# Kernel tuning notes

Hardware: AMD Instinct MI355X
Metric: run time of the kernel (lower is better)

Reference implementation:

```python
import jax, jax.numpy as jnp
import numpy as np
from math import sqrt

B, S, I, H, O, R = 32, 2048, 128, 512, 64, 1
ALPHA = 0.1


def setup_inputs() -> dict:
    key = jax.random.key(0)
    ks = jax.random.split(key, 7)
    x = jax.random.normal(ks[0], (B, S, I), dtype=jnp.float32)
    input_projective = jax.random.normal(ks[1], (H, R), dtype=jnp.float32) / sqrt(H)
    input_receptive = jax.random.normal(ks[2], (I, R), dtype=jnp.float32) / sqrt(I)
    rec_projective = jax.random.normal(ks[3], (H, R), dtype=jnp.float32) / sqrt(H)
    rec_receptive = jax.random.normal(ks[4], (H, R), dtype=jnp.float32) / sqrt(H)
    bound = 1.0 / sqrt(H)
    readout_w = jax.random.uniform(ks[5], (O, H), minval=-bound, maxval=bound, dtype=jnp.float32)
    readout_b = jax.random.uniform(ks[6], (O,), minval=-bound, maxval=bound, dtype=jnp.float32)
    return {
        "x": x,
        "input_projective": input_projective,
        "input_receptive": input_receptive,
        "rec_projective": rec_projective,
        "rec_receptive": rec_receptive,
        "readout_w": readout_w,
        "readout_b": readout_b,
    }


def reference(x, input_projective, input_receptive, rec_projective, rec_receptive, readout_w, readout_b):
    # Precompute input drive for all steps using the low-rank factorization:
    # x_in[b,s,h] = x[b,s,:] @ input_receptive @ input_projective.T
    x_in = jnp.einsum("bsi,ir,hr->bsh", x, input_receptive, input_projective)

    def step(h, xin_t):
        # r_in = (J @ h.T).T with J = P @ R.T  ->  h @ R @ P.T (low-rank)
        r_in = (h @ rec_receptive) @ rec_projective.T
        dh = -h + jax.nn.relu(r_in + xin_t)  # activation = nlfun (relu)
        h = h + ALPHA * dh                   # Euler hidden update
        out_t = h @ readout_w.T + readout_b
        return h, out_t

    h0 = jnp.zeros((x.shape[0], rec_projective.shape[0]), dtype=x.dtype)
    _, out = jax.lax.scan(step, h0, jnp.swapaxes(x_in, 0, 1))  # scan over time
    return jnp.swapaxes(out, 0, 1)  # [B, S, O]
```

## Files before the change

### kernel.cpp

```cpp
#include <hip/hip_runtime.h>


#define B_ 32
#define S_ 2048
#define I_ 128
#define H_ 512
#define O_ 64

typedef __attribute__((ext_vector_type(8))) short bf16x8;
typedef __attribute__((ext_vector_type(4))) float f32x4;

__device__ __forceinline__ unsigned short f2bf(float f) {
  unsigned int b = __float_as_uint(f);
  b += 0x7FFFu + ((b >> 16) & 1u);
  return (unsigned short)(b >> 16);
}
__device__ __forceinline__ float bf2f(unsigned short s) {
  return __uint_as_float(((unsigned)s) << 16);
}
__device__ __forceinline__ unsigned pack_bf(float lo, float hi) {
  unsigned a = (__float_as_uint(lo) + 0x8000u) >> 16;
  unsigned b = (__float_as_uint(hi) + 0x8000u) & 0xFFFF0000u;
  return a | b;
}

#define DPP_ADD(s, CTRL) \
  s += __int_as_float(__builtin_amdgcn_update_dpp(0, __float_as_int(s), CTRL, 0xF, 0xF, true))

#define RL(s, L) __int_as_float(__builtin_amdgcn_readlane(__float_as_int(s), (L)))

__device__ __forceinline__ void gload16(const void* g, void* l) {
  __builtin_amdgcn_global_load_lds(
      (const __attribute__((address_space(1))) unsigned int*)g,
      (__attribute__((address_space(3))) unsigned int*)l, 16, 0, 0);
}
#define WAITVM(N) asm volatile("s_waitcnt vmcnt(" #N ")" ::: "memory")
#define SCHEDB() __builtin_amdgcn_sched_barrier(0)

#define OFF_SU 0
#define OFF_SV 1920
#define OFF_RP 3456
#define OFF_IP 5504
#define OFF_SW 7552
#define OFF_XS 48512
#define SMEM_BYTES 146816

__device__ __forceinline__ int swz(int row, int col) {
  return row * 64 + (col ^ ((((unsigned)row >> 2) & 3) << 4));
}

__global__ __launch_bounds__(512, 1) void k_fused(
    const float* __restrict__ x, const float* __restrict__ ipj,
    const float* __restrict__ irc, const float* __restrict__ rpj,
    const float* __restrict__ rrc, const float* __restrict__ Wr,
    const float* __restrict__ bias, float* __restrict__ out) {
  extern __shared__ __align__(16) char smem[];
  float* su = (float*)(smem + OFF_SU);
  float* sV = (float*)(smem + OFF_SV);
  float* srp = (float*)(smem + OFF_RP);
  float* sip = (float*)(smem + OFF_IP);
  unsigned short* sw = (unsigned short*)(smem + OFF_SW);
  unsigned short* sBF = (unsigned short*)(smem + OFF_XS);
  float* xsf = (float*)(smem + OFF_XS);

  const int tid = threadIdx.x;
  const int wv = tid >> 6;
  const int lane = tid & 63;
  const int b = blockIdx.x >> 3;
  const int g = blockIdx.x & 7;
  const int r0 = g * 256;

  f32x4 cv0 = *(const f32x4*)(irc + 4 * (lane & 7));
  f32x4 cv1 = *(const f32x4*)(irc + 4 * (lane & 7) + 32);
  f32x4 cv2 = *(const f32x4*)(irc + 4 * (lane & 7) + 64);
  f32x4 cv3 = *(const f32x4*)(irc + 4 * (lane & 7) + 96);
  float rpv[8], ipv[8], rrv[8];
  #pragma unroll
  for (int k = 0; k < 8; k++) {
    int h = lane + 64 * k;
    rpv[k] = rpj[h]; ipv[k] = ipj[h]; rrv[k] = 0.1f * rrc[h];
  }
  if (tid < 96) su[384 + tid] = 0.f;
  if (tid < 80) sV[304 + tid] = 0.f;

#define ISSUE(c) do { \
    int tc_ = r0 - 128 + (c) * 64 + wv * 8; if (tc_ < 0) tc_ = 0; \
    const float* gs_ = x + ((size_t)b * S_ + tc_) * I_ + lane * 4; \
    char* ld_ = (char*)xsf + ((c) % 3) * 32768 + wv * 4096; \
    gload16(gs_,       ld_); \
    gload16(gs_ + 256, ld_ + 1024); \
    gload16(gs_ + 512, ld_ + 2048); \
    gload16(gs_ + 768, ld_ + 3072); \
  } while (0)

#define COMPUTE(c) do { \
    const float* bp_ = xsf + ((c) % 3) * 8192 + (wv * 8 + (lane >> 3)) * 128 + (lane & 7) * 4; \
    f32x4 x0_ = *(const f32x4*)(bp_); \
    f32x4 x1_ = *(const f32x4*)(bp_ + 32); \
    f32x4 x2_ = *(const f32x4*)(bp_ + 64); \
    f32x4 x3_ = *(const f32x4*)(bp_ + 96); \
    float p0_ = x0_[0] * cv0[0], p1_ = x0_[1] * cv0[1]; \
    float p2_ = x0_[2] * cv0[2], p3_ = x0_[3] * cv0[3]; \
    p0_ = fmaf(x1_[0], cv1[0], p0_); p1_ = fmaf(x1_[1], cv1[1], p1_); \
    p2_ = fmaf(x1_[2], cv1[2], p2_); p3_ = fmaf(x1_[3], cv1[3], p3_); \
    p0_ = fmaf(x2_[0], cv2[0], p0_); p1_ = fmaf(x2_[1], cv2[1], p1_); \
    p2_ = fmaf(x2_[2], cv2[2], p2_); p3_ = fmaf(x2_[3], cv2[3], p3_); \
    p0_ = fmaf(x3_[0], cv3[0], p0_); p1_ = fmaf(x3_[1], cv3[1], p1_); \
    p2_ = fmaf(x3_[2], cv3[2], p2_); p3_ = fmaf(x3_[3], cv3[3], p3_); \
    float s_ = (p0_ + p1_) + (p2_ + p3_); \
    DPP_ADD(s_, 0x121); DPP_ADD(s_, 0x122); DPP_ADD(s_, 0x124); \
    float mask_ = (r0 - 128 + (c) * 64 >= 0) ? 1.f : 0.f; \
    if ((lane & 7) == 7) su[(c) * 64 + wv * 8 + (lane >> 3)] = s_ * mask_; \
  } while (0)

  ISSUE(0); ISSUE(1); ISSUE(2);
  WAITVM(8); COMPUTE(0); SCHEDB(); ISSUE(3);
  WAITVM(8); COMPUTE(1); SCHEDB(); ISSUE(4);
  WAITVM(8); COMPUTE(2); SCHEDB(); ISSUE(5);
  WAITVM(8); COMPUTE(3);
  WAITVM(4); COMPUTE(4);
  WAITVM(0); COMPUTE(5);
  __syncthreads();

  if (wv < 4) {
    float suA = su[76 * wv + 32 + lane];
    float suB = su[76 * wv + 96 + lane];
#define VSTEP(UT) do { \
    float ut_ = (UT); \
    float q0 = fmaxf(fmaf(v, rpv[0], ut_ * ipv[0]), 0.f) * rrv[0]; \
    float q1 = fmaxf(fmaf(v, rpv[1], ut_ * ipv[1]), 0.f) * rrv[1]; \
    float q2 = fmaxf(fmaf(v, rpv[2], ut_ * ipv[2]), 0.f) * rrv[2]; \
    float q3 = fmaxf(fmaf(v, rpv[3], ut_ * ipv[3]), 0.f) * rrv[3]; \
    float q4 = fmaxf(fmaf(v, rpv[4], ut_ * ipv[4]), 0.f) * rrv[4]; \
    float q5 = fmaxf(fmaf(v, rpv[5], ut_ * ipv[5]), 0.f) * rrv[5]; \
    float q6 = fmaxf(fmaf(v, rpv[6], ut_ * ipv[6]), 0.f) * rrv[6]; \
    float q7 = fmaxf(fmaf(v, rpv[7], ut_ * ipv[7]), 0.f) * rrv[7]; \
    float s_ = ((q0 + q1) + (q2 + q3)) + ((q4 + q5) + (q6 + q7)); \
    DPP_ADD(s_, 0x121); DPP_ADD(s_, 0x122); DPP_ADD(s_, 0x124); DPP_ADD(s_, 0x128); \
    DPP_ADD(s_, 0x142); DPP_ADD(s_, 0x143); \
    float tot_ = RL(s_, 63); \
    v = fmaf(0.9f, v, tot_); \
  } while (0)
    float v = 0.f;
    int base = wv * 76;
    #pragma unroll 8
    for (int i = 0; i < 48; i++) VSTEP(RL(suA, i));
    #pragma unroll 8
    for (int k = 0; k < 16; k++) {
      if (lane == 0) sV[base + k] = v;
      VSTEP(RL(suA, 48 + k));
    }
    #pragma unroll 4
    for (int k = 16; k < 76; k++) {
      if (lane == 0) sV[base + k] = v;
      VSTEP(RL(suB, k - 16));
    }
  } else {
    int tid2 = tid - 256;
#define WSEG(m) do { \
    int seg_ = tid2 + 256 * (m); \
    int l2_ = seg_ & 63, ot_ = (seg_ >> 6) & 3, kt_ = seg_ >> 8; \
    const float4* wp_ = (const float4*)(Wr + (size_t)(ot_ * 16 + (l2_ & 15)) * H_ + kt_ * 32 + (l2_ >> 4) * 8); \
    float4 Wa_ = wp_[0], Wb_ = wp_[1]; \
    uint4 pk_; \
    pk_.x = (unsigned)f2bf(Wa_.x) | ((unsigned)f2bf(Wa_.y) << 16); \
    pk_.y = (unsigned)f2bf(Wa_.z) | ((unsigned)f2bf(Wa_.w) << 16); \
    pk_.z = (unsigned)f2bf(Wb_.x) | ((unsigned)f2bf(Wb_.y) << 16); \
    pk_.w = (unsigned)f2bf(Wb_.z) | ((unsigned)f2bf(Wb_.w) << 16); \
    *(uint4*)(sBF + seg_ * 8) = pk_; \
  } while (0)
    WSEG(0);  WSEG(1);  WSEG(2);  WSEG(3);
    WSEG(4);  WSEG(5);  WSEG(6);  WSEG(7);
    WSEG(8);  WSEG(9);  WSEG(10); WSEG(11);
    WSEG(12); WSEG(13); WSEG(14); WSEG(15);
    srp[tid2] = rpj[tid2]; srp[tid2 + 256] = rpj[tid2 + 256];
    sip[tid2] = ipj[tid2]; sip[tid2 + 256] = ipj[tid2 + 256];
  }
  __syncthreads();

  {
    int tl = lane & 15, quad = lane >> 4;
    float Vr0 = sV[(wv * 3 + 0) * 16 + tl], ur0 = su[80 + (wv * 3 + 0) * 16 + tl];
    float Vr1 = sV[(wv * 3 + 1) * 16 + tl], ur1 = su[80 + (wv * 3 + 1) * 16 + tl];
    float Vr2 = sV[(wv * 3 + 2) * 16 + tl], ur2 = su[80 + (wv * 3 + 2) * 16 + tl];
    f32x4 acc[3][4] = {};
    #pragma unroll 4
    for (int kt = 0; kt < 16; kt++) {
      int hbase = kt * 32 + quad * 8;
      f32x4 rp4a = *(const f32x4*)(srp + hbase);
      f32x4 rp4b = *(const f32x4*)(srp + hbase + 4);
      f32x4 ip4a = *(const f32x4*)(sip + hbase);
      f32x4 ip4b = *(const f32x4*)(sip + hbase + 4);
      bf16x8 bfr0 = *(const bf16x8*)(sBF + (((kt * 4 + 0) * 64 + lane) << 3));
      bf16x8 bfr1 = *(const bf16x8*)(sBF + (((kt * 4 + 1) * 64 + lane) << 3));
      bf16x8 bfr2 = *(const bf16x8*)(sBF + (((kt * 4 + 2) * 64 + lane) << 3));
      bf16x8 bfr3 = *(const bf16x8*)(sBF + (((kt * 4 + 3) * 64 + lane) << 3));
      #pragma unroll
      for (int m = 0; m < 3; m++) {
        float Vm = m == 0 ? Vr0 : (m == 1 ? Vr1 : Vr2);
        float um = m == 0 ? ur0 : (m == 1 ? ur1 : ur2);
        float q[8];
        #pragma unroll
        for (int j = 0; j < 4; j++) {
          q[j]     = fmaxf(fmaf(Vm, rp4a[j], um * ip4a[j]), 0.f);
          q[4 + j] = fmaxf(fmaf(Vm, rp4b[j], um * ip4b[j]), 0.f);
        }
        union { bf16x8 v; unsigned w[4]; } a;
        #pragma unroll
        for (int j = 0; j < 4; j++) a.w[j] = pack_bf(q[2 * j], q[2 * j + 1]);
        acc[m][0] = __builtin_amdgcn_mfma_f32_16x16x32_bf16(a.v, bfr0, acc[m][0], 0, 0, 0);
        acc[m][1] = __builtin_amdgcn_mfma_f32_16x16x32_bf16(a.v, bfr1, acc[m][1], 0, 0, 0);
        acc[m][2] = __builtin_amdgcn_mfma_f32_16x16x32_bf16(a.v, bfr2, acc[m][2], 0, 0, 0);
        acc[m][3] = __builtin_amdgcn_mfma_f32_16x16x32_bf16(a.v, bfr3, acc[m][3], 0, 0, 0);
      }
    }
    #pragma unroll
    for (int m = 0; m < 3; m++) {
      int mt = wv * 3 + m;
      if (mt < 19) {
        int rbase = mt * 16 + quad * 4;
        #pragma unroll
        for (int r = 0; r < 4; r++) {
          #pragma unroll
          for (int ot = 0; ot < 4; ot++)
            sw[swz(rbase + r, ot * 16 + tl)] = f2bf(acc[m][ot][r]);
        }
      }
    }
  }
  __syncthreads();

  {
    float y = 0.f;
    float bo = bias[lane];
    int k0 = wv * 32;
    float* ob = out + ((size_t)(b * S_ + r0 + k0)) * O_ + lane;
    #pragma unroll 8
    for (int i = 0; i < 48; i++)
      y = fmaf(0.9f, y, 0.1f * bf2f(sw[swz(k0 + i, lane)]));
    #pragma unroll 4
    for (int i = 0; i < 32; i++) {
      y = fmaf(0.9f, y, 0.1f * bf2f(sw[swz(k0 + 48 + i, lane)]));
      ob[(size_t)i * O_] = y + bo;
    }
  }
}

extern "C" void kernel_launch(void* const* d_in, const int* in_sizes, int n_in,
                              void* d_out, int out_size, void* d_ws, size_t ws_size,
                              hipStream_t stream) {
  const float* x   = (const float*)d_in[0];
  const float* ipj = (const float*)d_in[1];
  const float* irc = (const float*)d_in[2];
  const float* rpj = (const float*)d_in[3];
  const float* rrc = (const float*)d_in[4];
  const float* Wr  = (const float*)d_in[5];
  const float* br  = (const float*)d_in[6];
  float* out = (float*)d_out;

  static bool s_init = false;
  if (!s_init) {
    hipFuncSetAttribute((const void*)k_fused,
                        hipFuncAttributeMaxDynamicSharedMemorySize, SMEM_BYTES);
    s_init = true;
  }
  k_fused<<<dim3(256), dim3(512), SMEM_BYTES, stream>>>(x, ipj, irc, rpj, rrc,
                                                        Wr, br, out);
}
```

Before: 114.3 us.

## Fold scales into serial recurrence, use med3 clamp, inline DPP reduce and cvt_pk_bf16

The scalar recurrence now pre-multiplies the projective and input weights by 0.1*receptive, so the relu-then-scale becomes a single fmed3 clamp with sign-dependent bounds. The DPP reduction is written as inline v_add_f32_dpp asm, and bf16 packing uses the hardware v_cvt_pk_bf16_f32 instruction. The 0.1 factor in the readout scan moves to the output store. The warmup length of the serial scan drops from 48 to 32 steps, which shortens the latency-bound critical path but gives a shorter burn-in for each chunk's initial state and may reduce accuracy.

```diff
diff --git a/kernel.cpp b/kernel.cpp
--- a/kernel.cpp
+++ b/kernel.cpp
@@ -18,14 +18,23 @@
 __device__ __forceinline__ float bf2f(unsigned short s) {
   return __uint_as_float(((unsigned)s) << 16);
 }
-__device__ __forceinline__ unsigned pack_bf(float lo, float hi) {
-  unsigned a = (__float_as_uint(lo) + 0x8000u) >> 16;
-  unsigned b = (__float_as_uint(hi) + 0x8000u) & 0xFFFF0000u;
-  return a | b;
+__device__ __forceinline__ unsigned cvtpk(float lo, float hi) {
+  unsigned r;
+  asm("v_cvt_pk_bf16_f32 %0, %1, %2" : "=v"(r) : "v"(lo), "v"(hi));
+  return r;
 }
 
 #define DPP_ADD(s, CTRL) \
   s += __int_as_float(__builtin_amdgcn_update_dpp(0, __float_as_int(s), CTRL, 0xF, 0xF, true))
+
+#define DPP_RED(s) do { \
+  asm("v_add_f32_dpp %0, %0, %0 row_ror:1 row_mask:0xf bank_mask:0xf bound_ctrl:0" : "+v"(s)); \
+  asm("v_add_f32_dpp %0, %0, %0 row_ror:2 row_mask:0xf bank_mask:0xf bound_ctrl:0" : "+v"(s)); \
+  asm("v_add_f32_dpp %0, %0, %0 row_ror:4 row_mask:0xf bank_mask:0xf bound_ctrl:0" : "+v"(s)); \
+  asm("v_add_f32_dpp %0, %0, %0 row_ror:8 row_mask:0xf bank_mask:0xf bound_ctrl:0" : "+v"(s)); \
+  asm("v_add_f32_dpp %0, %0, %0 row_bcast:15 row_mask:0xa bank_mask:0xf" : "+v"(s)); \
+  asm("v_add_f32_dpp %0, %0, %0 row_bcast:31 row_mask:0xc bank_mask:0xf" : "+v"(s)); \
+} while (0)
 
 #define RL(s, L) __int_as_float(__builtin_amdgcn_readlane(__float_as_int(s), (L)))
 
@@ -74,11 +83,15 @@
   f32x4 cv1 = *(const f32x4*)(irc + 4 * (lane & 7) + 32);
   f32x4 cv2 = *(const f32x4*)(irc + 4 * (lane & 7) + 64);
   f32x4 cv3 = *(const f32x4*)(irc + 4 * (lane & 7) + 96);
-  float rpv[8], ipv[8], rrv[8];
+  float av[8], bv[8], lo_[8], hi_[8];
   #pragma unroll
   for (int k = 0; k < 8; k++) {
     int h = lane + 64 * k;
-    rpv[k] = rpj[h]; ipv[k] = ipj[h]; rrv[k] = 0.1f * rrc[h];
+    float rr = rrc[h], sc = 0.1f * rr;
+    av[k] = rpj[h] * sc;
+    bv[k] = ipj[h] * sc;
+    lo_[k] = rr > 0.f ? 0.f : -__builtin_inff();
+    hi_[k] = rr > 0.f ? __builtin_inff() : 0.f;
   }
   if (tid < 96) su[384 + tid] = 0.f;
   if (tid < 80) sV[304 + tid] = 0.f;
@@ -123,37 +136,44 @@
   __syncthreads();
 
   if (wv < 4) {
-    float suA = su[76 * wv + 32 + lane];
-    float suB = su[76 * wv + 96 + lane];
+    float suA = su[76 * wv + 48 + lane];
+    float suB = su[76 * wv + 112 + lane];
 #define VSTEP(UT) do { \
     float ut_ = (UT); \
-    float q0 = fmaxf(fmaf(v, rpv[0], ut_ * ipv[0]), 0.f) * rrv[0]; \
-    float q1 = fmaxf(fmaf(v, rpv[1], ut_ * ipv[1]), 0.f) * rrv[1]; \
-    float q2 = fmaxf(fmaf(v, rpv[2], ut_ * ipv[2]), 0.f) * rrv[2]; \
-    float q3 = fmaxf(fmaf(v, rpv[3], ut_ * ipv[3]), 0.f) * rrv[3]; \
-    float q4 = fmaxf(fmaf(v, rpv[4], ut_ * ipv[4]), 0.f) * rrv[4]; \
-    float q5 = fmaxf(fmaf(v, rpv[5], ut_ * ipv[5]), 0.f) * rrv[5]; \
-    float q6 = fmaxf(fmaf(v, rpv[6], ut_ * ipv[6]), 0.f) * rrv[6]; \
-    float q7 = fmaxf(fmaf(v, rpv[7], ut_ * ipv[7]), 0.f) * rrv[7]; \
+    float x0 = fmaf(v, av[0], ut_ * bv[0]); \
+    float x1 = fmaf(v, av[1], ut_ * bv[1]); \
+    float x2 = fmaf(v, av[2], ut_ * bv[2]); \
+    float x3 = fmaf(v, av[3], ut_ * bv[3]); \
+    float x4 = fmaf(v, av[4], ut_ * bv[4]); \
+    float x5 = fmaf(v, av[5], ut_ * bv[5]); \
+    float x6 = fmaf(v, av[6], ut_ * bv[6]); \
+    float x7 = fmaf(v, av[7], ut_ * bv[7]); \
+    float q0 = __builtin_amdgcn_fmed3f(x0, lo_[0], hi_[0]); \
+    float q1 = __builtin_amdgcn_fmed3f(x1, lo_[1], hi_[1]); \
+    float q2 = __builtin_amdgcn_fmed3f(x2, lo_[2], hi_[2]); \
+    float q3 = __builtin_amdgcn_fmed3f(x3, lo_[3], hi_[3]); \
+    float q4 = __builtin_amdgcn_fmed3f(x4, lo_[4], hi_[4]); \
+    float q5 = __builtin_amdgcn_fmed3f(x5, lo_[5], hi_[5]); \
+    float q6 = __builtin_amdgcn_fmed3f(x6, lo_[6], hi_[6]); \
+    float q7 = __builtin_amdgcn_fmed3f(x7, lo_[7], hi_[7]); \
     float s_ = ((q0 + q1) + (q2 + q3)) + ((q4 + q5) + (q6 + q7)); \
-    DPP_ADD(s_, 0x121); DPP_ADD(s_, 0x122); DPP_ADD(s_, 0x124); DPP_ADD(s_, 0x128); \
-    DPP_ADD(s_, 0x142); DPP_ADD(s_, 0x143); \
+    DPP_RED(s_); \
     float tot_ = RL(s_, 63); \
     v = fmaf(0.9f, v, tot_); \
   } while (0)
     float v = 0.f;
     int base = wv * 76;
     #pragma unroll 8
-    for (int i = 0; i < 48; i++) VSTEP(RL(suA, i));
+    for (int i = 0; i < 32; i++) VSTEP(RL(suA, i));
     #pragma unroll 8
-    for (int k = 0; k < 16; k++) {
+    for (int k = 0; k < 32; k++) {
       if (lane == 0) sV[base + k] = v;
-      VSTEP(RL(suA, 48 + k));
+      VSTEP(RL(suA, 32 + k));
     }
     #pragma unroll 4
-    for (int k = 16; k < 76; k++) {
+    for (int k = 32; k < 76; k++) {
       if (lane == 0) sV[base + k] = v;
-      VSTEP(RL(suB, k - 16));
+      VSTEP(RL(suB, k - 32));
     }
   } else {
     int tid2 = tid - 256;
@@ -163,10 +183,10 @@
     const float4* wp_ = (const float4*)(Wr + (size_t)(ot_ * 16 + (l2_ & 15)) * H_ + kt_ * 32 + (l2_ >> 4) * 8); \
     float4 Wa_ = wp_[0], Wb_ = wp_[1]; \
     uint4 pk_; \
-    pk_.x = (unsigned)f2bf(Wa_.x) | ((unsigned)f2bf(Wa_.y) << 16); \
-    pk_.y = (unsigned)f2bf(Wa_.z) | ((unsigned)f2bf(Wa_.w) << 16); \
-    pk_.z = (unsigned)f2bf(Wb_.x) | ((unsigned)f2bf(Wb_.y) << 16); \
-    pk_.w = (unsigned)f2bf(Wb_.z) | ((unsigned)f2bf(Wb_.w) << 16); \
+    pk_.x = cvtpk(Wa_.x, Wa_.y); \
+    pk_.y = cvtpk(Wa_.z, Wa_.w); \
+    pk_.z = cvtpk(Wb_.x, Wb_.y); \
+    pk_.w = cvtpk(Wb_.z, Wb_.w); \
     *(uint4*)(sBF + seg_ * 8) = pk_; \
   } while (0)
     WSEG(0);  WSEG(1);  WSEG(2);  WSEG(3);
@@ -207,7 +227,7 @@
         }
         union { bf16x8 v; unsigned w[4]; } a;
         #pragma unroll
-        for (int j = 0; j < 4; j++) a.w[j] = pack_bf(q[2 * j], q[2 * j + 1]);
+        for (int j = 0; j < 4; j++) a.w[j] = cvtpk(q[2 * j], q[2 * j + 1]);
         acc[m][0] = __builtin_amdgcn_mfma_f32_16x16x32_bf16(a.v, bfr0, acc[m][0], 0, 0, 0);
         acc[m][1] = __builtin_amdgcn_mfma_f32_16x16x32_bf16(a.v, bfr1, acc[m][1], 0, 0, 0);
         acc[m][2] = __builtin_amdgcn_mfma_f32_16x16x32_bf16(a.v, bfr2, acc[m][2], 0, 0, 0);
@@ -237,11 +257,11 @@
     float* ob = out + ((size_t)(b * S_ + r0 + k0)) * O_ + lane;
     #pragma unroll 8
     for (int i = 0; i < 48; i++)
-      y = fmaf(0.9f, y, 0.1f * bf2f(sw[swz(k0 + i, lane)]));
+      y = fmaf(0.9f, y, bf2f(sw[swz(k0 + i, lane)]));
     #pragma unroll 4
     for (int i = 0; i < 32; i++) {
-      y = fmaf(0.9f, y, 0.1f * bf2f(sw[swz(k0 + 48 + i, lane)]));
-      ob[(size_t)i * O_] = y + bo;
+      y = fmaf(0.9f, y, bf2f(sw[swz(k0 + 48 + i, lane)]));
+      ob[(size_t)i * O_] = fmaf(0.1f, y, bo);
     }
   }
 }
```

Measured after the change: 110.3 us. -3.6%, faster.
